# Kernel optimization log

Measured on AMD Instinct MI355X. Metric: run time of the kernel, lower is better.

## Reference

```python
import jax, jax.numpy as jnp
import numpy as np

BS, NCAMS, CIN, H, W = 4, 1, 256, 56, 200
MID = 128
DCH = 112  # (58-2)/0.5 depth bins
GX, GY, GZ = 128, 128, 16  # voxel grid


def setup_inputs() -> dict:
    key = jax.random.key(0)
    ks = jax.random.split(key, 32)
    f32 = jnp.float32

    def n(k, shape, scale=0.05):
        return jax.random.normal(k, shape, f32) * scale

    inp = {
        'img_feat': jax.random.normal(ks[0], (BS, NCAMS, CIN, H, W), f32),
        'scaled_pixel_size': jax.random.uniform(ks[1], (BS * NCAMS, 1), f32) * 2.0 + 0.5,
        # normalized sampling coords, slightly beyond [-1,1] to exercise zero padding
        'grids': jax.random.uniform(ks[2], (NCAMS, BS, GX, GY, GZ, 3), f32) * 2.2 - 1.1,
        # reduce_conv: Conv2d(CIN->MID,3x3,bias) + BN(affine, eval=per-channel scale/shift)
        'rc_w': n(ks[3], (MID, CIN, 3, 3)),
        'rc_b': n(ks[4], (MID,)),
        'rc_s': 1.0 + n(ks[5], (MID,)),
        'rc_t': n(ks[6], (MID,)),
        # Mlp(1 -> MID -> MID)
        'fc1_w': n(ks[7], (MID, 1), 0.5),
        'fc1_b': n(ks[8], (MID,)),
        'fc2_w': n(ks[9], (MID, MID)),
        'fc2_b': n(ks[10], (MID,)),
        # SELayer 1x1 convs (act on [N,MID,1,1] -> plain linears)
        'se_rw': n(ks[11], (MID, MID)),
        'se_rb': n(ks[12], (MID,)),
        'se_ew': n(ks[13], (MID, MID)),
        'se_eb': n(ks[14], (MID,)),
        # 3 BasicBlocks: conv3x3(no bias)+BN+ReLU+conv3x3(no bias)+BN, residual, ReLU
        'bb_w1': n(ks[15], (3, MID, MID, 3, 3)),
        'bb_s1': 1.0 + n(ks[16], (3, MID)),
        'bb_t1': n(ks[17], (3, MID)),
        'bb_w2': n(ks[18], (3, MID, MID, 3, 3)),
        'bb_s2': 1.0 + n(ks[19], (3, MID)),
        'bb_t2': n(ks[20], (3, MID)),
        # depth_pred 1x1 conv MID -> DCH
        'dp_w': n(ks[21], (DCH, MID)),
        'dp_b': n(ks[22], (DCH,)),
    }
    return inp


def _conv2d(x, w):
    return jax.lax.conv_general_dilated(x, w, (1, 1), 'SAME',
                                        dimension_numbers=('NCHW', 'OIHW', 'NCHW'))


def _aff(x, s, t):
    return x * s[None, :, None, None] + t[None, :, None, None]


def grid_sample_3d(feat, grid):
    """Trilinear grid_sample, zeros padding, align_corners=False.
    feat: [N,C,D,H,W]; grid: [N,X,Y,Z,3] with (x,y,z) in [-1,1] indexing (W,H,D).
    Returns [N,C,X,Y,Z]."""
    N, C, D, Hh, Ww = feat.shape
    ix = (grid[..., 0] + 1.0) * (Ww * 0.5) - 0.5
    iy = (grid[..., 1] + 1.0) * (Hh * 0.5) - 0.5
    iz = (grid[..., 2] + 1.0) * (D * 0.5) - 0.5
    x0 = jnp.floor(ix); y0 = jnp.floor(iy); z0 = jnp.floor(iz)
    fx, fy, fz = ix - x0, iy - y0, iz - z0

    def one(f, x0, y0, z0, fx, fy, fz):
        out = jnp.zeros((C,) + x0.shape, f.dtype)
        x0i = x0.astype(jnp.int32); y0i = y0.astype(jnp.int32); z0i = z0.astype(jnp.int32)
        for dz in (0, 1):
            for dy in (0, 1):
                for dx in (0, 1):
                    xi = x0i + dx; yi = y0i + dy; zi = z0i + dz
                    wgt = ((fx if dx else 1.0 - fx) * (fy if dy else 1.0 - fy)
                           * (fz if dz else 1.0 - fz))
                    valid = ((xi >= 0) & (xi < Ww) & (yi >= 0) & (yi < Hh)
                             & (zi >= 0) & (zi < D))
                    v = f[:, jnp.clip(zi, 0, D - 1), jnp.clip(yi, 0, Hh - 1),
                          jnp.clip(xi, 0, Ww - 1)]
                    out = out + v * (wgt * valid)[None]
        return out

    return jax.vmap(one)(feat, x0, y0, z0, fx, fy, fz)


def reference(img_feat, scaled_pixel_size, grids, rc_w, rc_b, rc_s, rc_t,
              fc1_w, fc1_b, fc2_w, fc2_b, se_rw, se_rb, se_ew, se_eb,
              bb_w1, bb_s1, bb_t1, bb_w2, bb_s2, bb_t2, dp_w, dp_b):
    bs, n_cams, c, h, w = img_feat.shape
    x = img_feat.reshape(bs * n_cams, c, h, w)
    # DepthNet (infer_mode): reduce_conv
    x = jax.nn.relu(_aff(_conv2d(x, rc_w) + rc_b[None, :, None, None], rc_s, rc_t))
    # Mlp on scaled_pixel_size + SE gating
    hmid = jax.nn.relu(scaled_pixel_size @ fc1_w.T + fc1_b) @ fc2_w.T + fc2_b
    se = jax.nn.relu(hmid @ se_rw.T + se_rb) @ se_ew.T + se_eb
    x = x * jax.nn.sigmoid(se)[:, :, None, None]
    # 3 BasicBlocks
    for i in range(3):
        y = jax.nn.relu(_aff(_conv2d(x, bb_w1[i]), bb_s1[i], bb_t1[i]))
        y = _aff(_conv2d(y, bb_w2[i]), bb_s2[i], bb_t2[i])
        x = jax.nn.relu(x + y)
    # depth_pred 1x1 conv, softmax over depth bins
    depth_feat = jnp.einsum('nchw,dc->ndhw', x, dp_w) + dp_b[None, :, None, None]
    depth = jax.nn.softmax(depth_feat, axis=1)
    depth = depth.reshape(bs, n_cams, 1, DCH, h, w)
    # per-camera frustum -> voxel bilinear sampling
    all_voxel_features = []
    for i in range(n_cams):
        all_voxel_features.append(grid_sample_3d(depth[:, i], grids[i]))
    agg = all_voxel_features[0]  # n_cams == 1 path in original forward
    return agg  # [bs, 1, GX, GY, GZ]
```

## Files before the change

kernel.cpp:

```cpp
#include <hip/hip_runtime.h>
#include <math.h>

typedef _Float16 v8h __attribute__((ext_vector_type(8)));
typedef float v4f __attribute__((ext_vector_type(4)));
typedef float v16f __attribute__((ext_vector_type(16)));

__global__ void __launch_bounds__(256) prep_kernel(
    const float* __restrict__ rc_w, const float* __restrict__ bb_w1,
    const float* __restrict__ bb_w2, const float* __restrict__ dp_w,
    const float* __restrict__ img, const float* __restrict__ sps,
    const float* __restrict__ fc1_w, const float* __restrict__ fc1_b,
    const float* __restrict__ fc2_w, const float* __restrict__ fc2_b,
    const float* __restrict__ se_rw, const float* __restrict__ se_rb,
    const float* __restrict__ se_ew, const float* __restrict__ se_eb,
    _Float16* __restrict__ wrc, _Float16* __restrict__ wbb,
    _Float16* __restrict__ wdp, _Float16* __restrict__ act16,
    float* __restrict__ sig) {
  const int bx = blockIdx.x;
  const int tid = threadIdx.x;
  __shared__ float buf[128];

  if (bx < 583) {
    int slot = bx * 256 + tid;
    if (slot < 36864) {
      int co = slot & 127;
      int r = slot >> 7;
      int kh = r & 1;
      r >>= 1;
      int tap = r % 9, c16 = r / 9;
      int cibase = c16 * 16 + kh * 8;
      v8h o;
#pragma unroll
      for (int j = 0; j < 8; ++j)
        o[j] = (_Float16)rc_w[((size_t)co * 256 + cibase + j) * 9 + tap];
      *(v8h*)(wrc + (size_t)slot * 8) = o;
    } else if (slot < 147456) {
      int s2 = slot - 36864;
      int blk = s2 / 18432, r2 = s2 - blk * 18432;
      int co = r2 & 127;
      int r = r2 >> 7;
      int kh = r & 1;
      r >>= 1;
      int tap = r % 9, c16 = r / 9;
      int cibase = c16 * 16 + kh * 8;
      const float* src = (blk < 3) ? (bb_w1 + (size_t)blk * 147456)
                                   : (bb_w2 + (size_t)(blk - 3) * 147456);
      int cslot = (blk < 3) ? (2 * blk) : (2 * (blk - 3) + 1);
      v8h o;
#pragma unroll
      for (int j = 0; j < 8; ++j)
        o[j] = (_Float16)src[((size_t)co * 128 + cibase + j) * 9 + tap];
      *(v8h*)(wbb + ((size_t)cslot * 18432 + r2) * 8) = o;
    } else if (slot < 149248) {
      int s3 = slot - 147456;
      v8h o;
#pragma unroll
      for (int j = 0; j < 8; ++j) o[j] = (_Float16)dp_w[(size_t)s3 * 8 + j];
      *(v8h*)(wdp + (size_t)s3 * 8) = o;
    }
  } else if (bx == 583) {
    const int j = tid;
    const bool on = j < 128;
    for (int b = 0; b < 4; ++b) {
      float h1 = 0.f;
      if (on) h1 = fmaxf(sps[b] * fc1_w[j] + fc1_b[j], 0.f);
      __syncthreads();
      if (on) buf[j] = h1;
      __syncthreads();
      float hm = 0.f;
      if (on) {
        hm = fc2_b[j];
        for (int k = 0; k < 128; ++k) hm += buf[k] * fc2_w[j * 128 + k];
      }
      __syncthreads();
      if (on) buf[j] = hm;
      __syncthreads();
      float t = 0.f;
      if (on) {
        t = se_rb[j];
        for (int k = 0; k < 128; ++k) t += buf[k] * se_rw[j * 128 + k];
        t = fmaxf(t, 0.f);
      }
      __syncthreads();
      if (on) buf[j] = t;
      __syncthreads();
      if (on) {
        float se = se_eb[j];
        for (int k = 0; k < 128; ++k) se += buf[k] * se_ew[j * 128 + k];
        sig[b * 128 + j] = 1.f / (1.f + expf(-se));
      }
      __syncthreads();
    }
  } else {
    const int bid = bx - 584;
    const int n = bid / 56, h = bid - n * 56;
    const int w = tid;
    if (w < 200) {
      const float* ip = img + ((size_t)n * 256 * 56 + h) * 200 + w;
      _Float16* op = act16 + (((size_t)n * 56 + h) * 200 + w) * 256;
#pragma unroll 4
      for (int c8 = 0; c8 < 32; ++c8) {
        v8h o;
#pragma unroll
        for (int j = 0; j < 8; ++j)
          o[j] = (_Float16)ip[(size_t)(c8 * 8 + j) * 11200];
        *(v8h*)(op + c8 * 8) = o;
      }
    }
  }
}

template <int CIN, int MODE>
__global__ void __launch_bounds__(512, 4) conv3x3_kernel(
    const _Float16* __restrict__ act, const _Float16* __restrict__ wr,
    const _Float16* __restrict__ xprev, const float* __restrict__ bias,
    const float* __restrict__ sc, const float* __restrict__ tr,
    const float* __restrict__ sig_se, _Float16* __restrict__ out) {
  constexpr int NCH = CIN / 16;
  const int wt = blockIdx.x, ht = blockIdx.y;
  const int n = blockIdx.z >> 1, cg = blockIdx.z & 1;
  const int h0 = ht * 8, w0 = wt * 32;
  const int tid = threadIdx.x;
  const int wave = tid >> 6, lane = tid & 63;
  const int l31 = lane & 31, khalf = lane >> 5;
  const int wv = wave >> 1, kc = wave & 1;

  __shared__ alignas(16) _Float16 ldsA[2][2 * 340 * 8];
  __shared__ alignas(16) _Float16 ldsB[2][1152 * 8];

  size_t goffA[2];
  int loffA[2];
  bool exA[2], okA[2];
#pragma unroll
  for (int it = 0; it < 2; ++it) {
    int slot = it * 512 + tid;
    int pos = slot >> 1, part = slot & 1;
    int hh = pos / 34, ww = pos - hh * 34;
    int gh = h0 - 1 + hh, gw = w0 - 1 + ww;
    exA[it] = slot < 680;
    bool inimg = (unsigned)gh < 56u && (unsigned)gw < 200u;
    okA[it] = exA[it] && inimg;
    loffA[it] = (part * 340 + pos) * 8;
    int ghc = okA[it] ? gh : 0, gwc = okA[it] ? gw : 0;
    goffA[it] = (((size_t)n * 56 + ghc) * 200 + gwc) * CIN + part * 8;
  }
  size_t goffB[3];
  int loffB[3];
  bool exB[3];
#pragma unroll
  for (int it = 0; it < 3; ++it) {
    int slot = it * 512 + tid;
    exB[it] = slot < 1152;
    int s = exB[it] ? slot : 0;
    int tap = s >> 7, kh = (s >> 6) & 1, co = s & 63;
    goffB[it] = (((size_t)(tap * 2 + kh)) * 128 + cg * 64 + co) * 8;
    loffB[it] = s * 8;
  }

  const v8h zero8 = {(_Float16)0, (_Float16)0, (_Float16)0, (_Float16)0,
                     (_Float16)0, (_Float16)0, (_Float16)0, (_Float16)0};
  v8h preA[2], preB[3];
#pragma unroll
  for (int it = 0; it < 2; ++it) preA[it] = okA[it] ? *(const v8h*)(act + goffA[it]) : zero8;
#pragma unroll
  for (int it = 0; it < 3; ++it) preB[it] = exB[it] ? *(const v8h*)(wr + goffB[it]) : zero8;

  v16f acc[2];
#pragma unroll
  for (int mt = 0; mt < 2; ++mt)
#pragma unroll
    for (int r = 0; r < 16; ++r) acc[mt][r] = 0.f;

#pragma unroll 1
  for (int c = 0; c < NCH; ++c) {
    _Float16* aB = &ldsA[c & 1][0];
    _Float16* bB = &ldsB[c & 1][0];
#pragma unroll
    for (int it = 0; it < 2; ++it)
      if (exA[it]) *(v8h*)(aB + loffA[it]) = preA[it];
#pragma unroll
    for (int it = 0; it < 3; ++it)
      if (exB[it]) *(v8h*)(bB + loffB[it]) = preB[it];
    __syncthreads();
    if (c + 1 < NCH) {
#pragma unroll
      for (int it = 0; it < 2; ++it)
        preA[it] = okA[it] ? *(const v8h*)(act + goffA[it] + (size_t)(c + 1) * 16) : zero8;
#pragma unroll
      for (int it = 0; it < 3; ++it)
        preB[it] = exB[it] ? *(const v8h*)(wr + goffB[it] + (size_t)(c + 1) * 18432) : zero8;
    }
#pragma unroll
    for (int dy = 0; dy < 3; ++dy) {
#pragma unroll
      for (int dx = 0; dx < 3; ++dx) {
        const int tap = dy * 3 + dx;
        v8h bfrag = *(const v8h*)(bB + (tap * 128 + khalf * 64 + kc * 32 + l31) * 8);
#pragma unroll
        for (int mt = 0; mt < 2; ++mt) {
          const int pos = (wv * 2 + mt + dy) * 34 + l31 + dx;
          v8h afrag = *(const v8h*)(aB + (khalf * 340 + pos) * 8);
          acc[mt] = __builtin_amdgcn_mfma_f32_32x32x16_f16(afrag, bfrag, acc[mt], 0, 0, 0);
        }
      }
    }
  }

#pragma unroll
  for (int mt = 0; mt < 2; ++mt) {
    const int h = h0 + wv * 2 + mt;
    const int cc = cg * 64 + kc * 32 + l31;
    const float s = sc[cc], t = tr[cc];
    float bb = 0.f, sg = 1.f;
    if constexpr (MODE == 0) {
      bb = bias[cc];
      sg = sig_se[n * 128 + cc];
    }
#pragma unroll
    for (int r = 0; r < 16; ++r) {
      const int m = (r & 3) + 8 * (r >> 2) + 4 * khalf;
      const int w = w0 + m;
      if (w < 200) {
        float v = acc[mt][r];
        size_t oidx = (((size_t)n * 56 + h) * 200 + w) * 128 + cc;
        if constexpr (MODE == 0) v = fmaxf((v + bb) * s + t, 0.f) * sg;
        if constexpr (MODE == 1) v = fmaxf(v * s + t, 0.f);
        if constexpr (MODE == 2) v = fmaxf((float)xprev[oidx] + v * s + t, 0.f);
        out[oidx] = (_Float16)v;
      }
    }
  }
}

__global__ void __launch_bounds__(256) depth_proj_softmax_kernel(
    const _Float16* __restrict__ x, const _Float16* __restrict__ wdp,
    const float* __restrict__ dp_b, _Float16* __restrict__ depth) {
  const int wave = threadIdx.x >> 6, lane = threadIdx.x & 63;
  const int q = lane >> 4, l16 = lane & 15;
  const int pos0 = blockIdx.x * 64 + wave * 16;

  v4f acc[7];
#pragma unroll
  for (int nt = 0; nt < 7; ++nt) {
    float bv = dp_b[nt * 16 + l16];
    acc[nt] = {bv, bv, bv, bv};
  }
#pragma unroll
  for (int c0 = 0; c0 < 128; c0 += 32) {
    v8h a = *(const v8h*)(x + (size_t)(pos0 + l16) * 128 + c0 + q * 8);
#pragma unroll
    for (int nt = 0; nt < 7; ++nt) {
      v8h b = *(const v8h*)(wdp + (size_t)(nt * 16 + l16) * 128 + c0 + q * 8);
      acc[nt] = __builtin_amdgcn_mfma_f32_16x16x32_f16(a, b, acc[nt], 0, 0, 0);
    }
  }
  float m[4];
#pragma unroll
  for (int r = 0; r < 4; ++r) {
    m[r] = acc[0][r];
#pragma unroll
    for (int nt = 1; nt < 7; ++nt) m[r] = fmaxf(m[r], acc[nt][r]);
  }
#pragma unroll
  for (int off = 1; off < 16; off <<= 1)
#pragma unroll
    for (int r = 0; r < 4; ++r) m[r] = fmaxf(m[r], __shfl_xor(m[r], off));
  float s[4] = {0.f, 0.f, 0.f, 0.f};
#pragma unroll
  for (int nt = 0; nt < 7; ++nt)
#pragma unroll
    for (int r = 0; r < 4; ++r) {
      float e = expf(acc[nt][r] - m[r]);
      acc[nt][r] = e;
      s[r] += e;
    }
#pragma unroll
  for (int off = 1; off < 16; off <<= 1)
#pragma unroll
    for (int r = 0; r < 4; ++r) s[r] += __shfl_xor(s[r], off);
#pragma unroll
  for (int r = 0; r < 4; ++r) {
    const float inv = 1.f / s[r];
    const size_t p = pos0 + q * 4 + r;
#pragma unroll
    for (int nt = 0; nt < 7; ++nt)
      depth[p * 112 + nt * 16 + l16] = (_Float16)(acc[nt][r] * inv);
  }
}

__global__ void __launch_bounds__(256) gridsample_kernel(
    const float* __restrict__ grids, const _Float16* __restrict__ depth,
    float* __restrict__ out) {
  const int i = blockIdx.x * 256 + threadIdx.x;
  const int n = i >> 18;
  const float gx = grids[(size_t)i * 3];
  const float gy = grids[(size_t)i * 3 + 1];
  const float gz = grids[(size_t)i * 3 + 2];
  const float ix = (gx + 1.f) * 100.f - 0.5f;
  const float iy = (gy + 1.f) * 28.f - 0.5f;
  const float iz = (gz + 1.f) * 56.f - 0.5f;
  const float xf = floorf(ix), yf = floorf(iy), zf = floorf(iz);
  const int x0 = (int)xf, y0 = (int)yf, z0 = (int)zf;
  const float fx = ix - xf, fy = iy - yf, fz = iz - zf;
  const bool zv0 = (unsigned)z0 < 112u;
  const bool zv1 = (unsigned)(z0 + 1) < 112u;
  const float wz0 = 1.f - fz, wz1 = fz;
  float acc = 0.f;
#pragma unroll
  for (int dy = 0; dy < 2; ++dy) {
    const int yi = y0 + dy;
    const float wy = dy ? fy : 1.f - fy;
#pragma unroll
    for (int dx = 0; dx < 2; ++dx) {
      const int xi = x0 + dx;
      const float wx = dx ? fx : 1.f - fx;
      if ((unsigned)xi < 200u && (unsigned)yi < 56u) {
        const _Float16* bp = depth + ((size_t)n * 11200 + yi * 200 + xi) * 112;
        float v0 = zv0 ? (float)bp[z0] : 0.f;
        float v1 = zv1 ? (float)bp[z0 + 1] : 0.f;
        acc += (wx * wy) * (wz0 * v0 + wz1 * v1);
      }
    }
  }
  out[i] = acc;
}

extern "C" void kernel_launch(void* const* d_in, const int* in_sizes, int n_in,
                              void* d_out, int out_size, void* d_ws, size_t ws_size,
                              hipStream_t stream) {
  (void)in_sizes; (void)n_in; (void)out_size; (void)ws_size;
  const float* img = (const float*)d_in[0];
  const float* sps = (const float*)d_in[1];
  const float* grids = (const float*)d_in[2];
  const float* rc_w = (const float*)d_in[3];
  const float* rc_b = (const float*)d_in[4];
  const float* rc_s = (const float*)d_in[5];
  const float* rc_t = (const float*)d_in[6];
  const float* fc1_w = (const float*)d_in[7];
  const float* fc1_b = (const float*)d_in[8];
  const float* fc2_w = (const float*)d_in[9];
  const float* fc2_b = (const float*)d_in[10];
  const float* se_rw = (const float*)d_in[11];
  const float* se_rb = (const float*)d_in[12];
  const float* se_ew = (const float*)d_in[13];
  const float* se_eb = (const float*)d_in[14];
  const float* bb_w1 = (const float*)d_in[15];
  const float* bb_s1 = (const float*)d_in[16];
  const float* bb_t1 = (const float*)d_in[17];
  const float* bb_w2 = (const float*)d_in[18];
  const float* bb_s2 = (const float*)d_in[19];
  const float* bb_t2 = (const float*)d_in[20];
  const float* dp_w = (const float*)d_in[21];
  const float* dp_b = (const float*)d_in[22];
  float* outp = (float*)d_out;

  char* ws = (char*)d_ws;
  _Float16* act16 = (_Float16*)(ws + 0);
  _Float16* depth16 = (_Float16*)(ws + 0);
  _Float16* xa = (_Float16*)(ws + 23068672);
  _Float16* xb = (_Float16*)(ws + 23068672 + 11534336);
  _Float16* yb = (_Float16*)(ws + 23068672 + 2 * 11534336);
  _Float16* wrc = (_Float16*)(ws + 57671680);
  _Float16* wdp = (_Float16*)(ws + 57671680 + 589824);
  _Float16* wbb = (_Float16*)(ws + 58327040);
  float* sig = (float*)(ws + 58327040 + 1769472);

  prep_kernel<<<dim3(808), 256, 0, stream>>>(
      rc_w, bb_w1, bb_w2, dp_w, img, sps, fc1_w, fc1_b, fc2_w, fc2_b, se_rw, se_rb,
      se_ew, se_eb, wrc, wbb, wdp, act16, sig);

  dim3 cgrid(7, 7, 8);
  conv3x3_kernel<256, 0><<<cgrid, 512, 0, stream>>>(act16, wrc, nullptr, rc_b, rc_s,
                                                    rc_t, sig, xa);
  _Float16* xcur = xa;
  _Float16* xnxt = xb;
  for (int i = 0; i < 3; ++i) {
    conv3x3_kernel<128, 1><<<cgrid, 512, 0, stream>>>(
        xcur, wbb + (size_t)(2 * i) * 147456, nullptr, nullptr, bb_s1 + i * 128,
        bb_t1 + i * 128, nullptr, yb);
    conv3x3_kernel<128, 2><<<cgrid, 512, 0, stream>>>(
        yb, wbb + (size_t)(2 * i + 1) * 147456, xcur, nullptr, bb_s2 + i * 128,
        bb_t2 + i * 128, nullptr, xnxt);
    _Float16* t = xcur;
    xcur = xnxt;
    xnxt = t;
  }

  depth_proj_softmax_kernel<<<dim3(700), 256, 0, stream>>>(xcur, wdp, dp_b, depth16);
  gridsample_kernel<<<dim3(4096), 256, 0, stream>>>(grids, depth16, outp);
}
```

Before: 409.2 us.

## Split conv output channels into quarters and stage weight repack through LDS

```diff
diff --git a/kernel.cpp b/kernel.cpp
--- a/kernel.cpp
+++ b/kernel.cpp
@@ -18,81 +18,106 @@
     float* __restrict__ sig) {
   const int bx = blockIdx.x;
   const int tid = threadIdx.x;
-  __shared__ float buf[128];
-
-  if (bx < 583) {
-    int slot = bx * 256 + tid;
-    if (slot < 36864) {
-      int co = slot & 127;
-      int r = slot >> 7;
-      int kh = r & 1;
-      r >>= 1;
-      int tap = r % 9, c16 = r / 9;
-      int cibase = c16 * 16 + kh * 8;
-      v8h o;
-#pragma unroll
-      for (int j = 0; j < 8; ++j)
-        o[j] = (_Float16)rc_w[((size_t)co * 256 + cibase + j) * 9 + tap];
-      *(v8h*)(wrc + (size_t)slot * 8) = o;
-    } else if (slot < 147456) {
-      int s2 = slot - 36864;
-      int blk = s2 / 18432, r2 = s2 - blk * 18432;
-      int co = r2 & 127;
-      int r = r2 >> 7;
-      int kh = r & 1;
-      r >>= 1;
-      int tap = r % 9, c16 = r / 9;
-      int cibase = c16 * 16 + kh * 8;
-      const float* src = (blk < 3) ? (bb_w1 + (size_t)blk * 147456)
-                                   : (bb_w2 + (size_t)(blk - 3) * 147456);
-      int cslot = (blk < 3) ? (2 * blk) : (2 * (blk - 3) + 1);
-      v8h o;
-#pragma unroll
-      for (int j = 0; j < 8; ++j)
-        o[j] = (_Float16)src[((size_t)co * 128 + cibase + j) * 9 + tap];
-      *(v8h*)(wbb + ((size_t)cslot * 18432 + r2) * 8) = o;
-    } else if (slot < 149248) {
-      int s3 = slot - 147456;
-      v8h o;
-#pragma unroll
-      for (int j = 0; j < 8; ++j) o[j] = (_Float16)dp_w[(size_t)s3 * 8 + j];
-      *(v8h*)(wdp + (size_t)s3 * 8) = o;
-    }
-  } else if (bx == 583) {
+  __shared__ float lds[9224];
+
+  if (bx < 32) {
+    const float* src = rc_w + (size_t)bx * 4 * 2304;
+#pragma unroll
+    for (int r = 0; r < 36; ++r) {
+      int e = r * 256 + tid;
+      int col = e / 2304;
+      int rem = e - col * 2304;
+      lds[col * 2305 + rem] = src[e];
+    }
+    __syncthreads();
+#pragma unroll
+    for (int ro = 0; ro < 5; ++ro) {
+      int lidx = ro * 256 + tid;
+      if (lidx < 1152) {
+        int col = lidx & 3;
+        int r = lidx >> 2;
+        int kh = r & 1;
+        int ct = r >> 1;
+        int tap = ct % 9, c16 = ct / 9;
+        v8h o;
+#pragma unroll
+        for (int j = 0; j < 8; ++j)
+          o[j] = (_Float16)lds[col * 2305 + (c16 * 16 + kh * 8 + j) * 9 + tap];
+        *(v8h*)(wrc + ((size_t)r * 128 + bx * 4 + col) * 8) = o;
+      }
+    }
+  } else if (bx < 128) {
+    const int t = bx - 32;
+    const int k = t >> 4, g = t & 15;
+    const float* base = (k < 3) ? (bb_w1 + (size_t)k * 147456)
+                                : (bb_w2 + (size_t)(k - 3) * 147456);
+    const int cslot = (k < 3) ? (2 * k) : (2 * (k - 3) + 1);
+    const float* src = base + (size_t)g * 8 * 1152;
+#pragma unroll
+    for (int r = 0; r < 36; ++r) {
+      int e = r * 256 + tid;
+      int col = e / 1152;
+      int rem = e - col * 1152;
+      lds[col * 1153 + rem] = src[e];
+    }
+    __syncthreads();
+#pragma unroll
+    for (int ro = 0; ro < 5; ++ro) {
+      int lidx = ro * 256 + tid;
+      if (lidx < 1152) {
+        int col = lidx & 7;
+        int r = lidx >> 3;
+        int kh = r & 1;
+        int ct = r >> 1;
+        int tap = ct % 9, c16 = ct / 9;
+        v8h o;
+#pragma unroll
+        for (int j = 0; j < 8; ++j)
+          o[j] = (_Float16)lds[col * 1153 + (c16 * 16 + kh * 8 + j) * 9 + tap];
+        *(v8h*)(wbb + (size_t)cslot * 147456 + ((size_t)r * 128 + g * 8 + col) * 8) = o;
+      }
+    }
+  } else if (bx < 135) {
+    int s3 = (bx - 128) * 256 + tid;
+    v8h o;
+#pragma unroll
+    for (int j = 0; j < 8; ++j) o[j] = (_Float16)dp_w[(size_t)s3 * 8 + j];
+    *(v8h*)(wdp + (size_t)s3 * 8) = o;
+  } else if (bx == 135) {
     const int j = tid;
     const bool on = j < 128;
     for (int b = 0; b < 4; ++b) {
       float h1 = 0.f;
       if (on) h1 = fmaxf(sps[b] * fc1_w[j] + fc1_b[j], 0.f);
       __syncthreads();
-      if (on) buf[j] = h1;
+      if (on) lds[j] = h1;
       __syncthreads();
       float hm = 0.f;
       if (on) {
         hm = fc2_b[j];
-        for (int k = 0; k < 128; ++k) hm += buf[k] * fc2_w[j * 128 + k];
-      }
-      __syncthreads();
-      if (on) buf[j] = hm;
+        for (int k = 0; k < 128; ++k) hm += lds[k] * fc2_w[j * 128 + k];
+      }
+      __syncthreads();
+      if (on) lds[j] = hm;
       __syncthreads();
       float t = 0.f;
       if (on) {
         t = se_rb[j];
-        for (int k = 0; k < 128; ++k) t += buf[k] * se_rw[j * 128 + k];
+        for (int k = 0; k < 128; ++k) t += lds[k] * se_rw[j * 128 + k];
         t = fmaxf(t, 0.f);
       }
       __syncthreads();
-      if (on) buf[j] = t;
+      if (on) lds[j] = t;
       __syncthreads();
       if (on) {
         float se = se_eb[j];
-        for (int k = 0; k < 128; ++k) se += buf[k] * se_ew[j * 128 + k];
+        for (int k = 0; k < 128; ++k) se += lds[k] * se_ew[j * 128 + k];
         sig[b * 128 + j] = 1.f / (1.f + expf(-se));
       }
       __syncthreads();
     }
   } else {
-    const int bid = bx - 584;
+    const int bid = bx - 136;
     const int n = bid / 56, h = bid - n * 56;
     const int w = tid;
     if (w < 200) {
@@ -111,29 +136,29 @@
 }
 
 template <int CIN, int MODE>
-__global__ void __launch_bounds__(512, 4) conv3x3_kernel(
+__global__ void __launch_bounds__(256, 4) conv3x3_kernel(
     const _Float16* __restrict__ act, const _Float16* __restrict__ wr,
     const _Float16* __restrict__ xprev, const float* __restrict__ bias,
     const float* __restrict__ sc, const float* __restrict__ tr,
     const float* __restrict__ sig_se, _Float16* __restrict__ out) {
   constexpr int NCH = CIN / 16;
   const int wt = blockIdx.x, ht = blockIdx.y;
-  const int n = blockIdx.z >> 1, cg = blockIdx.z & 1;
+  const int n = blockIdx.z >> 2, cq = blockIdx.z & 3;
   const int h0 = ht * 8, w0 = wt * 32;
   const int tid = threadIdx.x;
   const int wave = tid >> 6, lane = tid & 63;
   const int l31 = lane & 31, khalf = lane >> 5;
-  const int wv = wave >> 1, kc = wave & 1;
+  const int wv = wave;
 
   __shared__ alignas(16) _Float16 ldsA[2][2 * 340 * 8];
-  __shared__ alignas(16) _Float16 ldsB[2][1152 * 8];
-
-  size_t goffA[2];
-  int loffA[2];
-  bool exA[2], okA[2];
-#pragma unroll
-  for (int it = 0; it < 2; ++it) {
-    int slot = it * 512 + tid;
+  __shared__ alignas(16) _Float16 ldsB[2][576 * 8];
+
+  size_t goffA[3];
+  int loffA[3];
+  bool exA[3], okA[3];
+#pragma unroll
+  for (int it = 0; it < 3; ++it) {
+    int slot = it * 256 + tid;
     int pos = slot >> 1, part = slot & 1;
     int hh = pos / 34, ww = pos - hh * 34;
     int gh = h0 - 1 + hh, gw = w0 - 1 + ww;
@@ -149,19 +174,19 @@
   bool exB[3];
 #pragma unroll
   for (int it = 0; it < 3; ++it) {
-    int slot = it * 512 + tid;
-    exB[it] = slot < 1152;
+    int slot = it * 256 + tid;
+    exB[it] = slot < 576;
     int s = exB[it] ? slot : 0;
-    int tap = s >> 7, kh = (s >> 6) & 1, co = s & 63;
-    goffB[it] = (((size_t)(tap * 2 + kh)) * 128 + cg * 64 + co) * 8;
+    int tap = s >> 6, kh = (s >> 5) & 1, co = s & 31;
+    goffB[it] = (((size_t)(tap * 2 + kh)) * 128 + cq * 32 + co) * 8;
     loffB[it] = s * 8;
   }
 
   const v8h zero8 = {(_Float16)0, (_Float16)0, (_Float16)0, (_Float16)0,
                      (_Float16)0, (_Float16)0, (_Float16)0, (_Float16)0};
-  v8h preA[2], preB[3];
-#pragma unroll
-  for (int it = 0; it < 2; ++it) preA[it] = okA[it] ? *(const v8h*)(act + goffA[it]) : zero8;
+  v8h preA[3], preB[3];
+#pragma unroll
+  for (int it = 0; it < 3; ++it) preA[it] = okA[it] ? *(const v8h*)(act + goffA[it]) : zero8;
 #pragma unroll
   for (int it = 0; it < 3; ++it) preB[it] = exB[it] ? *(const v8h*)(wr + goffB[it]) : zero8;
 
@@ -176,7 +201,7 @@
     _Float16* aB = &ldsA[c & 1][0];
     _Float16* bB = &ldsB[c & 1][0];
 #pragma unroll
-    for (int it = 0; it < 2; ++it)
+    for (int it = 0; it < 3; ++it)
       if (exA[it]) *(v8h*)(aB + loffA[it]) = preA[it];
 #pragma unroll
     for (int it = 0; it < 3; ++it)
@@ -184,7 +209,7 @@
     __syncthreads();
     if (c + 1 < NCH) {
 #pragma unroll
-      for (int it = 0; it < 2; ++it)
+      for (int it = 0; it < 3; ++it)
         preA[it] = okA[it] ? *(const v8h*)(act + goffA[it] + (size_t)(c + 1) * 16) : zero8;
 #pragma unroll
       for (int it = 0; it < 3; ++it)
@@ -195,7 +220,7 @@
 #pragma unroll
       for (int dx = 0; dx < 3; ++dx) {
         const int tap = dy * 3 + dx;
-        v8h bfrag = *(const v8h*)(bB + (tap * 128 + khalf * 64 + kc * 32 + l31) * 8);
+        v8h bfrag = *(const v8h*)(bB + (tap * 64 + khalf * 32 + l31) * 8);
 #pragma unroll
         for (int mt = 0; mt < 2; ++mt) {
           const int pos = (wv * 2 + mt + dy) * 34 + l31 + dx;
@@ -209,7 +234,7 @@
 #pragma unroll
   for (int mt = 0; mt < 2; ++mt) {
     const int h = h0 + wv * 2 + mt;
-    const int cc = cg * 64 + kc * 32 + l31;
+    const int cc = cq * 32 + l31;
     const float s = sc[cc], t = tr[cc];
     float bb = 0.f, sg = 1.f;
     if constexpr (MODE == 0) {
@@ -365,20 +390,20 @@
   _Float16* wbb = (_Float16*)(ws + 58327040);
   float* sig = (float*)(ws + 58327040 + 1769472);
 
-  prep_kernel<<<dim3(808), 256, 0, stream>>>(
+  prep_kernel<<<dim3(360), 256, 0, stream>>>(
       rc_w, bb_w1, bb_w2, dp_w, img, sps, fc1_w, fc1_b, fc2_w, fc2_b, se_rw, se_rb,
       se_ew, se_eb, wrc, wbb, wdp, act16, sig);
 
-  dim3 cgrid(7, 7, 8);
-  conv3x3_kernel<256, 0><<<cgrid, 512, 0, stream>>>(act16, wrc, nullptr, rc_b, rc_s,
+  dim3 cgrid(7, 7, 16);
+  conv3x3_kernel<256, 0><<<cgrid, 256, 0, stream>>>(act16, wrc, nullptr, rc_b, rc_s,
                                                     rc_t, sig, xa);
   _Float16* xcur = xa;
   _Float16* xnxt = xb;
   for (int i = 0; i < 3; ++i) {
-    conv3x3_kernel<128, 1><<<cgrid, 512, 0, stream>>>(
+    conv3x3_kernel<128, 1><<<cgrid, 256, 0, stream>>>(
         xcur, wbb + (size_t)(2 * i) * 147456, nullptr, nullptr, bb_s1 + i * 128,
         bb_t1 + i * 128, nullptr, yb);
-    conv3x3_kernel<128, 2><<<cgrid, 512, 0, stream>>>(
+    conv3x3_kernel<128, 2><<<cgrid, 256, 0, stream>>>(
         yb, wbb + (size_t)(2 * i + 1) * 147456, xcur, nullptr, bb_s2 + i * 128,
         bb_t2 + i * 128, nullptr, xnxt);
     _Float16* t = xcur;
```

Measured after the change: 418.6 us. +2.3%, slower.
